# Performance work log

Hardware: AMD Instinct MI355X
Metric: run time of the kernel (lower is better)

## Reference

```python
import jax, jax.numpy as jnp
import numpy as np

ALPHA = 0.2       # LeakyReLU negative slope
NEG = -9.0e15     # masking value used by the torch module

def setup_inputs() -> dict:
    key = jax.random.key(0)
    k1, k2, k3, k4, k5, k6 = jax.random.split(key, 6)
    bs, N, F_out, Fx = 32, 1024, 128, 8
    inputs = {
        "input": jax.random.normal(k1, (bs, N, 1), dtype=jnp.float32),
        "adj": jax.random.randint(k2, (N, N), 0, 2, dtype=jnp.int32),
        "ext_input": jax.random.normal(k3, (bs, N, Fx), dtype=jnp.float32),
        "side_input": jax.random.normal(k4, (bs, N, 1), dtype=jnp.float32),
        "W": jax.random.normal(k5, (1, F_out), dtype=jnp.float32) * (1.414 * (6.0 / (1 + F_out)) ** 0.5),
        "a": jax.random.normal(k6, (2 * F_out, 1), dtype=jnp.float32) * (1.414 * (6.0 / (2 * F_out + 1)) ** 0.5),
    }
    return inputs

def reference(input, adj, ext_input, side_input, W, a):
    # ext_input / side_input are reshaped but unused in the original forward.
    bs = input.shape[0]
    x = input.reshape(bs, -1, 1)                      # (bs, N, 1)
    h = jnp.matmul(x, W)                              # (bs, N, F)
    Fo = W.shape[1]
    a1 = a[:Fo, 0]                                    # (F,)
    a2 = a[Fo:, 0]                                    # (F,)
    # Decomposed concat-score: e[b,i,j] = leakyrelu(h_i . a1 + h_j . a2)
    s1 = jnp.einsum('bnf,f->bn', h, a1)               # (bs, N)
    s2 = jnp.einsum('bnf,f->bn', h, a2)               # (bs, N)
    e = jax.nn.leaky_relu(s1[:, :, None] + s2[:, None, :], negative_slope=ALPHA)  # (bs, N, N)
    mask = (adj > 0)[None, :, :]                      # broadcast over batch (adj.repeat)
    att = jnp.where(mask, e, NEG)
    att = jnp.where(att > 0, att, NEG)                # second positivity mask in the module
    att = jax.nn.softmax(att, axis=2)                 # (bs, N, N)
    h_prime = jnp.matmul(att, h)                      # (bs, N, F)
    return jax.nn.elu(h_prime)                        # concat=True branch
```

## Files before the change

### kernel.cpp

```cpp
#include <hip/hip_runtime.h>

constexpr int N  = 1024;
constexpr int BS = 32;
constexpr int FO = 128;

__global__ void prep_kernel(const float* __restrict__ W, const float* __restrict__ a,
                            float* __restrict__ ws) {
  int t = threadIdx.x;
  float p1 = W[t] * a[t]       + W[t + 64] * a[t + 64];
  float p2 = W[t] * a[FO + t]  + W[t + 64] * a[FO + 64 + t];
#pragma unroll
  for (int o = 32; o > 0; o >>= 1) {
    p1 += __shfl_xor(p1, o);
    p2 += __shfl_xor(p2, o);
  }
  if (t == 0) { ws[0] = p1; ws[1] = p2; }
}

__global__ void sums_kernel(const float* __restrict__ x, float* __restrict__ ws) {
  int b = blockIdx.x;
  int t = threadIdx.x;
  const float* xb = x + b * N;
  float p = xb[t] + xb[t + 256] + xb[t + 512] + xb[t + 768];
#pragma unroll
  for (int o = 32; o > 0; o >>= 1) p += __shfl_xor(p, o);
  __shared__ float sb[4];
  if ((t & 63) == 0) sb[t >> 6] = p;
  __syncthreads();
  if (t == 0) ws[2 + b] = sb[0] + sb[1] + sb[2] + sb[3];
}

__global__ __launch_bounds__(64) void gat_main(
    const float* __restrict__ x, const int* __restrict__ adj,
    const float* __restrict__ W, const float* __restrict__ ws,
    float* __restrict__ out) {
  const int i    = blockIdx.x;
  const int lane = threadIdx.x;
  const float c1 = ws[0], c2 = ws[1];

  float adjf[16];
  const int4* arow = reinterpret_cast<const int4*>(adj + (size_t)i * N);
#pragma unroll
  for (int k = 0; k < 4; ++k) {
    int4 aq = arow[lane + 64 * k];
    adjf[k * 4 + 0] = aq.x > 0 ? 1.f : 0.f;
    adjf[k * 4 + 1] = aq.y > 0 ? 1.f : 0.f;
    adjf[k * 4 + 2] = aq.z > 0 ? 1.f : 0.f;
    adjf[k * 4 + 3] = aq.w > 0 ? 1.f : 0.f;
  }
  const float wlo = W[lane], whi = W[lane + 64];

  const int b0 = blockIdx.y * (BS / 4);
  for (int b = b0; b < b0 + BS / 4; ++b) {
    const float* xb = x + b * N;
    const float thr = -c1 * xb[i];
    float Z = 0.f, Wm = 0.f;
    const float4* xrow = reinterpret_cast<const float4*>(xb);
#pragma unroll
    for (int k = 0; k < 4; ++k) {
      float4 xq = xrow[lane + 64 * k];
      float xv[4] = {xq.x, xq.y, xq.z, xq.w};
#pragma unroll
      for (int m = 0; m < 4; ++m) {
        float w = c2 * xv[m];
        float u = __expf(w);
        float keep = (w > thr) ? adjf[k * 4 + m] : 0.f;
        float uu = u * keep;
        Z += uu;
        Wm = fmaf(uu, xv[m], Wm);
      }
    }
#pragma unroll
    for (int o = 32; o > 0; o >>= 1) {
      Z  += __shfl_xor(Z, o);
      Wm += __shfl_xor(Wm, o);
    }
    float t = (Z > 0.f) ? (Wm / Z) : (ws[2 + b] * (1.f / N));

    float z0 = t * wlo, z1 = t * whi;
    float r0 = z0 > 0.f ? z0 : __expf(z0) - 1.f;
    float r1 = z1 > 0.f ? z1 : __expf(z1) - 1.f;
    float* orow = out + ((size_t)b * N + i) * FO;
    orow[lane]      = r0;
    orow[lane + 64] = r1;
  }
}

extern "C" void kernel_launch(void* const* d_in, const int* in_sizes, int n_in,
                              void* d_out, int out_size, void* d_ws, size_t ws_size,
                              hipStream_t stream) {
  const float* x   = (const float*)d_in[0];
  const int*   adj = (const int*)d_in[1];
  const float* W   = (const float*)d_in[4];
  const float* a   = (const float*)d_in[5];
  float* out = (float*)d_out;
  float* ws  = (float*)d_ws;

  hipLaunchKernelGGL(prep_kernel, dim3(1), dim3(64), 0, stream, W, a, ws);
  hipLaunchKernelGGL(sums_kernel, dim3(BS), dim3(256), 0, stream, x, ws);
  hipLaunchKernelGGL(gat_main, dim3(N, 4), dim3(64), 0, stream, x, adj, W, ws, out);
}
```

Before: 85.15 us.

## Fuse prep and sum kernels into main GAT kernel with DPP reductions

Removes the separate prep and per-batch sum kernels by computing the W·a dot products and the row sum of x inside each block, so only one kernel is launched. Wave reductions switch from shfl_xor to DPP row operations plus a readlane broadcast, and the output store becomes one float2 per lane. Each block now recomputes the dot products redundantly and does an extra sum reduction per batch.

Result: no change. 83.84 us (-1.5%).

```diff
diff --git a/kernel.cpp b/kernel.cpp
--- a/kernel.cpp
+++ b/kernel.cpp
@@ -4,39 +4,34 @@
 constexpr int BS = 32;
 constexpr int FO = 128;
 
-__global__ void prep_kernel(const float* __restrict__ W, const float* __restrict__ a,
-                            float* __restrict__ ws) {
-  int t = threadIdx.x;
-  float p1 = W[t] * a[t]       + W[t + 64] * a[t + 64];
-  float p2 = W[t] * a[FO + t]  + W[t + 64] * a[FO + 64 + t];
-#pragma unroll
-  for (int o = 32; o > 0; o >>= 1) {
-    p1 += __shfl_xor(p1, o);
-    p2 += __shfl_xor(p2, o);
-  }
-  if (t == 0) { ws[0] = p1; ws[1] = p2; }
+template <int ctrl, int rmask>
+__device__ __forceinline__ float dpp_add(float x) {
+  int y = __builtin_amdgcn_update_dpp(0, __float_as_int(x), ctrl, rmask, 0xf, true);
+  return x + __int_as_float(y);
 }
 
-__global__ void sums_kernel(const float* __restrict__ x, float* __restrict__ ws) {
-  int b = blockIdx.x;
-  int t = threadIdx.x;
-  const float* xb = x + b * N;
-  float p = xb[t] + xb[t + 256] + xb[t + 512] + xb[t + 768];
-#pragma unroll
-  for (int o = 32; o > 0; o >>= 1) p += __shfl_xor(p, o);
-  __shared__ float sb[4];
-  if ((t & 63) == 0) sb[t >> 6] = p;
-  __syncthreads();
-  if (t == 0) ws[2 + b] = sb[0] + sb[1] + sb[2] + sb[3];
+__device__ __forceinline__ float wave_sum_bcast(float x) {
+  x = dpp_add<0x111, 0xf>(x);
+  x = dpp_add<0x112, 0xf>(x);
+  x = dpp_add<0x114, 0xf>(x);
+  x = dpp_add<0x118, 0xf>(x);
+  x = dpp_add<0x142, 0xa>(x);
+  x = dpp_add<0x143, 0xc>(x);
+  return __int_as_float(__builtin_amdgcn_readlane(__float_as_int(x), 63));
 }
 
-__global__ __launch_bounds__(64) void gat_main(
+__global__ __launch_bounds__(64) void gat_fused(
     const float* __restrict__ x, const int* __restrict__ adj,
-    const float* __restrict__ W, const float* __restrict__ ws,
+    const float* __restrict__ W, const float* __restrict__ a,
     float* __restrict__ out) {
   const int i    = blockIdx.x;
   const int lane = threadIdx.x;
-  const float c1 = ws[0], c2 = ws[1];
+
+  const float wl = W[lane], wh = W[lane + 64];
+  const float c1 = wave_sum_bcast(wl * a[lane] + wh * a[lane + 64]);
+  const float c2 = wave_sum_bcast(wl * a[FO + lane] + wh * a[FO + 64 + lane]);
+
+  const float2 w2 = reinterpret_cast<const float2*>(W)[lane];
 
   float adjf[16];
   const int4* arow = reinterpret_cast<const int4*>(adj + (size_t)i * N);
@@ -48,13 +43,12 @@
     adjf[k * 4 + 2] = aq.z > 0 ? 1.f : 0.f;
     adjf[k * 4 + 3] = aq.w > 0 ? 1.f : 0.f;
   }
-  const float wlo = W[lane], whi = W[lane + 64];
 
   const int b0 = blockIdx.y * (BS / 4);
   for (int b = b0; b < b0 + BS / 4; ++b) {
     const float* xb = x + b * N;
     const float thr = -c1 * xb[i];
-    float Z = 0.f, Wm = 0.f;
+    float Z = 0.f, Wm = 0.f, S = 0.f;
     const float4* xrow = reinterpret_cast<const float4*>(xb);
 #pragma unroll
     for (int k = 0; k < 4; ++k) {
@@ -62,27 +56,25 @@
       float xv[4] = {xq.x, xq.y, xq.z, xq.w};
 #pragma unroll
       for (int m = 0; m < 4; ++m) {
-        float w = c2 * xv[m];
+        float xj = xv[m];
+        S += xj;
+        float w = c2 * xj;
         float u = __expf(w);
-        float keep = (w > thr) ? adjf[k * 4 + m] : 0.f;
-        float uu = u * keep;
+        float uu = ((w > thr) ? adjf[k * 4 + m] : 0.f) * u;
         Z += uu;
-        Wm = fmaf(uu, xv[m], Wm);
+        Wm = fmaf(uu, xj, Wm);
       }
     }
-#pragma unroll
-    for (int o = 32; o > 0; o >>= 1) {
-      Z  += __shfl_xor(Z, o);
-      Wm += __shfl_xor(Wm, o);
-    }
-    float t = (Z > 0.f) ? (Wm / Z) : (ws[2 + b] * (1.f / N));
+    Z  = wave_sum_bcast(Z);
+    Wm = wave_sum_bcast(Wm);
+    S  = wave_sum_bcast(S);
+    float t = (Z > 0.f) ? (Wm / Z) : (S * (1.f / N));
 
-    float z0 = t * wlo, z1 = t * whi;
-    float r0 = z0 > 0.f ? z0 : __expf(z0) - 1.f;
-    float r1 = z1 > 0.f ? z1 : __expf(z1) - 1.f;
-    float* orow = out + ((size_t)b * N + i) * FO;
-    orow[lane]      = r0;
-    orow[lane + 64] = r1;
+    float z0 = t * w2.x, z1 = t * w2.y;
+    float2 r;
+    r.x = z0 > 0.f ? z0 : __expf(z0) - 1.f;
+    r.y = z1 > 0.f ? z1 : __expf(z1) - 1.f;
+    reinterpret_cast<float2*>(out + ((size_t)b * N + i) * FO)[lane] = r;
   }
 }
 
@@ -94,9 +86,7 @@
   const float* W   = (const float*)d_in[4];
   const float* a   = (const float*)d_in[5];
   float* out = (float*)d_out;
-  float* ws  = (float*)d_ws;
 
-  hipLaunchKernelGGL(prep_kernel, dim3(1), dim3(64), 0, stream, W, a, ws);
-  hipLaunchKernelGGL(sums_kernel, dim3(BS), dim3(256), 0, stream, x, ws);
-  hipLaunchKernelGGL(gat_main, dim3(N, 4), dim3(64), 0, stream, x, adj, W, ws, out);
+  hipLaunchKernelGGL(gat_fused, dim3(N, 4), dim3(64), 0, stream,
+                     x, adj, W, a, out);
 }
```
